# Performance work log

Hardware: AMD Instinct MI355X
Metric: run time of the kernel (lower is better)

The kernel has to match this reference:

```python
import jax, jax.numpy as jnp
import numpy as np

B, SEQ, IN, H = 256, 128, 512, 512


def setup_inputs() -> dict:
    key = jax.random.key(0)
    ks = jax.random.split(key, 7)
    s = 1.0 / np.sqrt(H)  # torch LSTM/Linear default init scale
    return {
        "x": jax.random.normal(ks[0], (B, SEQ, IN), dtype=jnp.float32),
        "W_ih": jax.random.uniform(ks[1], (4 * H, IN), jnp.float32, -s, s),
        "W_hh": jax.random.uniform(ks[2], (4 * H, H), jnp.float32, -s, s),
        "b_ih": jax.random.uniform(ks[3], (4 * H,), jnp.float32, -s, s),
        "b_hh": jax.random.uniform(ks[4], (4 * H,), jnp.float32, -s, s),
        "Wa": jax.random.uniform(ks[5], (SEQ, H), jnp.float32, -s, s),
        "ba": jax.random.uniform(ks[6], (SEQ,), jnp.float32, -s, s),
    }


def _lstm_cell(xi, h, c, W_ih, W_hh, b):
    # torch gate order: input, forget, cell(g), output
    gates = xi @ W_ih.T + h @ W_hh.T + b  # [B, 4H]
    i, f, g, o = jnp.split(gates, 4, axis=-1)
    c_new = jax.nn.sigmoid(f) * c + jax.nn.sigmoid(i) * jnp.tanh(g)
    h_new = jax.nn.sigmoid(o) * jnp.tanh(c_new)
    return h_new, c_new


def reference(x, W_ih, W_hh, b_ih, b_hh, Wa, ba):
    b = b_ih + b_hh
    bs, seq = x.shape[0], Wa.shape[0]
    h = jnp.zeros((bs, W_hh.shape[1]), x.dtype)
    c = jnp.zeros_like(h)
    # initial step on zero input (x[:,0]*0), zero initial state
    h, c = _lstm_cell(jnp.zeros((bs, x.shape[2]), x.dtype), h, c, W_ih, W_hh, b)

    def step(carry, _):
        h, c = carry
        attn = jax.nn.softmax(c @ Wa.T + ba, axis=-1)      # [B, seq]
        xi = jnp.einsum('bs,bsd->bd', attn, x)             # attention-weighted input
        h, c = _lstm_cell(xi, h, c, W_ih, W_hh, b)
        return (h, c), h

    _, hs = jax.lax.scan(step, (h, c), None, length=seq)   # [seq, B, H]
    return jnp.transpose(hs, (1, 0, 2))                    # [B, seq, H]
```

## Files before the change

kernel.cpp:

```cpp
#include <hip/hip_runtime.h>
#include <stdint.h>

#define BDIM 256
#define SEQL 128
#define IND 512
#define HID 512
#define KDIM 1024

typedef __bf16 bf16x8 __attribute__((ext_vector_type(8)));
typedef float floatx4 __attribute__((ext_vector_type(4)));
typedef _Float16 f16x8 __attribute__((ext_vector_type(8)));

__device__ __forceinline__ float sigm(float x) { return 1.0f / (1.0f + __expf(-x)); }

__device__ __forceinline__ ushort f2bf(float v) {
  uint32_t x = __builtin_bit_cast(uint32_t, v);
  x += 0x7fffu + ((x >> 16) & 1u);
  return (ushort)(x >> 16);
}
__device__ __forceinline__ float bf2f(ushort u) {
  return __builtin_bit_cast(float, ((uint32_t)u) << 16);
}

__global__ __launch_bounds__(256) void k_wconv(
    const float* __restrict__ W_ih, const float* __restrict__ W_hh,
    const float* __restrict__ b_ih, const float* __restrict__ b_hh,
    ushort* __restrict__ Whi, ushort* __restrict__ Wlo, float* __restrict__ bias) {
  int row = blockIdx.x;
  if (threadIdx.x == 0) bias[row] = b_ih[row] + b_hh[row];
  for (int k = threadIdx.x; k < KDIM; k += 256) {
    float w = (k < IND) ? W_ih[(size_t)row * IND + k] : W_hh[(size_t)row * HID + (k - IND)];
    ushort hi = f2bf(w);
    Whi[(size_t)row * KDIM + k] = hi;
    Wlo[(size_t)row * KDIM + k] = f2bf(w - bf2f(hi));
  }
}

__global__ __launch_bounds__(256) void k_xconv(const float* __restrict__ x,
                                               _Float16* __restrict__ xh) {
  size_t i = ((size_t)blockIdx.x * 256 + threadIdx.x) * 8;
  float4 v0 = *(const float4*)(x + i);
  float4 v1 = *(const float4*)(x + i + 4);
  f16x8 o;
  o[0] = (_Float16)v0.x; o[1] = (_Float16)v0.y; o[2] = (_Float16)v0.z; o[3] = (_Float16)v0.w;
  o[4] = (_Float16)v1.x; o[5] = (_Float16)v1.y; o[6] = (_Float16)v1.z; o[7] = (_Float16)v1.w;
  *(f16x8*)(xh + i) = o;
}

__global__ void k_init(const float* __restrict__ b_ih, const float* __restrict__ b_hh,
                       float* __restrict__ c, ushort* __restrict__ Ahi, ushort* __restrict__ Alo) {
  int b = blockIdx.x;
  for (int j = threadIdx.x; j < HID; j += blockDim.x) {
    float bi = b_ih[j] + b_hh[j];
    float bg = b_ih[2 * HID + j] + b_hh[2 * HID + j];
    float bo = b_ih[3 * HID + j] + b_hh[3 * HID + j];
    float c0 = sigm(bi) * tanhf(bg);
    float h0 = sigm(bo) * tanhf(c0);
    c[b * HID + j] = c0;
    ushort hi = f2bf(h0);
    Ahi[(size_t)b * KDIM + IND + j] = hi;
    Alo[(size_t)b * KDIM + IND + j] = f2bf(h0 - bf2f(hi));
  }
}

__global__ __launch_bounds__(256) void k_attn(const float* __restrict__ c, const float* __restrict__ Wa,
                                              const float* __restrict__ ba, const _Float16* __restrict__ xh,
                                              ushort* __restrict__ Ahi, ushort* __restrict__ Alo) {
  __shared__ float sc[HID];
  __shared__ float sl[SEQL];
  __shared__ float sxi[4][HID];
  int b = blockIdx.x, tid = threadIdx.x;
  sc[tid] = c[b * HID + tid];
  sc[tid + 256] = c[b * HID + tid + 256];
  __syncthreads();
  int wave = tid >> 6, lane = tid & 63;
  float4 c0 = *(const float4*)(&sc[lane * 4]);
  float4 c1 = *(const float4*)(&sc[lane * 4 + 256]);
#pragma unroll 4
  for (int si = 0; si < 32; ++si) {
    int s = wave * 32 + si;
    const float4* wr = (const float4*)(Wa + (size_t)s * HID);
    float4 w0 = wr[lane];
    float4 w1 = wr[lane + 64];
    float acc = c0.x * w0.x + c0.y * w0.y + c0.z * w0.z + c0.w * w0.w
              + c1.x * w1.x + c1.y * w1.y + c1.z * w1.z + c1.w * w1.w;
#pragma unroll
    for (int off = 32; off > 0; off >>= 1) acc += __shfl_down(acc, off);
    if (lane == 0) sl[s] = acc + ba[s];
  }
  __syncthreads();
  if (tid < 64) {
    float v0 = sl[tid], v1 = sl[tid + 64];
    float m = fmaxf(v0, v1);
#pragma unroll
    for (int off = 32; off > 0; off >>= 1) m = fmaxf(m, __shfl_xor(m, off));
    float e0 = __expf(v0 - m), e1 = __expf(v1 - m);
    float s2 = e0 + e1;
#pragma unroll
    for (int off = 32; off > 0; off >>= 1) s2 += __shfl_xor(s2, off);
    float inv = 1.f / s2;
    sl[tid] = e0 * inv; sl[tid + 64] = e1 * inv;
  }
  __syncthreads();
  int cix = tid & 63;
  int qp = tid >> 6;
  const _Float16* xrow = xh + (size_t)b * SEQL * IND + (size_t)qp * 32 * IND + 8 * cix;
  float a0 = 0.f, a1 = 0.f, a2 = 0.f, a3 = 0.f, a4 = 0.f, a5 = 0.f, a6 = 0.f, a7 = 0.f;
#pragma unroll 8
  for (int s = 0; s < 32; ++s) {
    float w = sl[qp * 32 + s];
    f16x8 v = *(const f16x8*)(xrow + (size_t)s * IND);
    a0 += w * (float)v[0]; a1 += w * (float)v[1];
    a2 += w * (float)v[2]; a3 += w * (float)v[3];
    a4 += w * (float)v[4]; a5 += w * (float)v[5];
    a6 += w * (float)v[6]; a7 += w * (float)v[7];
  }
  *(float4*)(&sxi[qp][8 * cix])     = (float4){a0, a1, a2, a3};
  *(float4*)(&sxi[qp][8 * cix + 4]) = (float4){a4, a5, a6, a7};
  __syncthreads();
  float rx = sxi[0][2 * tid] + sxi[1][2 * tid] + sxi[2][2 * tid] + sxi[3][2 * tid];
  float ry = sxi[0][2 * tid + 1] + sxi[1][2 * tid + 1] + sxi[2][2 * tid + 1] + sxi[3][2 * tid + 1];
  ushort hx = f2bf(rx), hy = f2bf(ry);
  uint hp = (uint)hx | ((uint)hy << 16);
  uint lp = (uint)f2bf(rx - bf2f(hx)) | ((uint)f2bf(ry - bf2f(hy)) << 16);
  *(uint*)(Ahi + (size_t)b * KDIM + 2 * tid) = hp;
  *(uint*)(Alo + (size_t)b * KDIM + 2 * tid) = lp;
}

#define G3LOAD(R, KO) do { \
  R##a  = *(const uint4*)(gA + (KO)); \
  R##w0 = *(const uint4*)(gWhi + (KO));      R##w1 = *(const uint4*)(gWhi + (KO) + 8);  \
  R##w2 = *(const uint4*)(gWlo + (KO));      R##w3 = *(const uint4*)(gWlo + (KO) + 8);  } while (0)
#define G3STORE(BUF, R) do { \
  *(uint4*)&sA[BUF][sthalf][ar][ac] = R##a; \
  *(uint4*)&sW[BUF][0][wr][wc] = R##w0;  *(uint4*)&sW[BUF][0][wr][wc + 8] = R##w1; \
  *(uint4*)&sW[BUF][1][wr][wc] = R##w2;  *(uint4*)&sW[BUF][1][wr][wc + 8] = R##w3; } while (0)
#define G3COMPUTE(BUF) do { \
  _Pragma("unroll") for (int ks = 0; ks < 2; ++ks) { \
    int kb = ks * 32 + koff; \
    bf16x8 ah = *(const bf16x8*)(&sA[BUF][0][ml][kb]); \
    bf16x8 al = *(const bf16x8*)(&sA[BUF][1][ml][kb]); \
    bf16x8 wh = *(const bf16x8*)(&sW[BUF][0][g * 16 + ml][kb]); \
    bf16x8 wl = *(const bf16x8*)(&sW[BUF][1][g * 16 + ml][kb]); \
    accA = __builtin_amdgcn_mfma_f32_16x16x32_bf16(ah, wh, accA, 0, 0, 0); \
    accB = __builtin_amdgcn_mfma_f32_16x16x32_bf16(ah, wl, accB, 0, 0, 0); \
    accB = __builtin_amdgcn_mfma_f32_16x16x32_bf16(al, wh, accB, 0, 0, 0); } } while (0)

__global__ __launch_bounds__(256) void k_gates(
    const ushort* __restrict__ Whi, const ushort* __restrict__ Wlo,
    const float* __restrict__ bias,
    const ushort* __restrict__ Ahi, const ushort* __restrict__ Alo,
    float* __restrict__ c, float* __restrict__ out,
    ushort* __restrict__ Dhi, ushort* __restrict__ Dlo, int tstep) {
  int bid = blockIdx.x;
  int lb = (bid & 7) * 64 + (bid >> 3);
  int j0 = (lb >> 4) * 16;
  int b0 = (lb & 15) * 16;

  __shared__ __align__(16) ushort sA[2][2][16][72];
  __shared__ __align__(16) ushort sW[2][2][64][72];
  __shared__ float sR[4][16][16];

  int tid = threadIdx.x;
  int sthalf = tid >> 7;
  int ar = (tid & 127) >> 3;
  int ac = (tid & 7) * 8;
  const ushort* gA = (sthalf ? Alo : Ahi) + (size_t)(b0 + ar) * KDIM + ac;
  int wr = tid >> 2;
  int wc = (tid & 3) * 16;
  int wrow = (wr >> 4) * HID + j0 + (wr & 15);
  const ushort* gWhi = Whi + (size_t)wrow * KDIM + wc;
  const ushort* gWlo = Wlo + (size_t)wrow * KDIM + wc;

  floatx4 accA = {0.f, 0.f, 0.f, 0.f}, accB = {0.f, 0.f, 0.f, 0.f};
  int lane = tid & 63, g = tid >> 6;
  int ml = lane & 15;
  int koff = (lane >> 4) * 8;

  uint4 Aa, Aw0, Aw1, Aw2, Aw3;
  uint4 Ba, Bw0, Bw1, Bw2, Bw3;

  G3LOAD(A, 0);
  G3LOAD(B, 64);
  G3STORE(0, A);
  G3STORE(1, B);
  G3LOAD(A, 128);
  G3LOAD(B, 192);
  __syncthreads();

  for (int k0 = 0; k0 < 16; k0 += 2) {
    G3COMPUTE(0);
    __syncthreads();
    if (k0 + 2 < 16) {
      G3STORE(0, A);
      if (k0 + 4 < 16) G3LOAD(A, (k0 + 4) * 64);
    }
    G3COMPUTE(1);
    __syncthreads();
    if (k0 + 3 < 16) {
      G3STORE(1, B);
      if (k0 + 5 < 16) G3LOAD(B, (k0 + 5) * 64);
    }
  }

  {
    floatx4 acc = accA + accB;
#pragma unroll
    for (int r = 0; r < 4; ++r) sR[g][ml][(lane >> 4) * 4 + r] = acc[r];
  }
  __syncthreads();

  {
    int jj = tid & 15, bb = tid >> 4;
    int jg = j0 + jj;
    int b = b0 + bb;
    float ig = sigm(sR[0][jj][bb] + bias[jg]);
    float fg = sigm(sR[1][jj][bb] + bias[HID + jg]);
    float gg = tanhf(sR[2][jj][bb] + bias[2 * HID + jg]);
    float og = sigm(sR[3][jj][bb] + bias[3 * HID + jg]);
    float co = c[b * HID + jg];
    float cn = fg * co + ig * gg;
    float hv = og * tanhf(cn);
    c[b * HID + jg] = cn;
    out[((size_t)b * SEQL + tstep) * HID + jg] = hv;
    ushort hi = f2bf(hv);
    Dhi[(size_t)b * KDIM + IND + jg] = hi;
    Dlo[(size_t)b * KDIM + IND + jg] = f2bf(hv - bf2f(hi));
  }
}

extern "C" void kernel_launch(void* const* d_in, const int* in_sizes, int n_in,
                              void* d_out, int out_size, void* d_ws, size_t ws_size,
                              hipStream_t stream) {
  (void)in_sizes; (void)n_in; (void)out_size; (void)ws_size;
  const float* x    = (const float*)d_in[0];
  const float* W_ih = (const float*)d_in[1];
  const float* W_hh = (const float*)d_in[2];
  const float* b_ih = (const float*)d_in[3];
  const float* b_hh = (const float*)d_in[4];
  const float* Wa   = (const float*)d_in[5];
  const float* ba   = (const float*)d_in[6];
  float* out = (float*)d_out;

  char* p = (char*)d_ws;
  auto carve = [&](size_t bytes) { char* r = p; p += (bytes + 255) & ~(size_t)255; return r; };
  float*  c    = (float*)carve((size_t)BDIM * HID * 4);
  float*  bias = (float*)carve((size_t)4 * HID * 4);
  ushort* Whi  = (ushort*)carve((size_t)4 * HID * KDIM * 2);
  ushort* Wlo  = (ushort*)carve((size_t)4 * HID * KDIM * 2);
  ushort* A0hi = (ushort*)carve((size_t)BDIM * KDIM * 2);
  ushort* A0lo = (ushort*)carve((size_t)BDIM * KDIM * 2);
  ushort* A1hi = (ushort*)carve((size_t)BDIM * KDIM * 2);
  ushort* A1lo = (ushort*)carve((size_t)BDIM * KDIM * 2);
  _Float16* xh = (_Float16*)carve((size_t)BDIM * SEQL * IND * 2);

  k_wconv<<<4 * HID, 256, 0, stream>>>(W_ih, W_hh, b_ih, b_hh, Whi, Wlo, bias);
  k_xconv<<<(BDIM * SEQL * IND) / (256 * 8), 256, 0, stream>>>(x, xh);
  k_init<<<BDIM, 256, 0, stream>>>(b_ih, b_hh, c, A0hi, A0lo);

  for (int t = 0; t < SEQL; ++t) {
    ushort* Rhi = (t & 1) ? A1hi : A0hi;
    ushort* Rlo = (t & 1) ? A1lo : A0lo;
    ushort* Dhi = (t & 1) ? A0hi : A1hi;
    ushort* Dlo = (t & 1) ? A0lo : A1lo;
    k_attn<<<BDIM, 256, 0, stream>>>(c, Wa, ba, xh, Rhi, Rlo);
    k_gates<<<512, 256, 0, stream>>>(Whi, Wlo, bias, Rhi, Rlo, c, out, Dhi, Dlo, t);
  }
}
```

Baseline: 4.707 ms.

## Fuse attention and gate kernels per step with per-tile atomic barrier

Merges the per-timestep attention kernel and gate GEMM kernel into one launch of 256 blocks. Each block first computes the attention-weighted input for one batch row. It then waits on an atomic counter shared by the 16 blocks of its batch tile, and finally computes gates for 16 batch rows by 32 hidden units. The aim is to halve kernel launches and the gaps between them, and to halve reloads of the activation tile by doubling each block's weight tile. The cost is a spin barrier that assumes all blocks are co-resident, plus fewer blocks for the GEMM phase.

```diff
diff --git a/kernel.cpp b/kernel.cpp
--- a/kernel.cpp
+++ b/kernel.cpp
@@ -63,169 +63,198 @@
   }
 }
 
-__global__ __launch_bounds__(256) void k_attn(const float* __restrict__ c, const float* __restrict__ Wa,
-                                              const float* __restrict__ ba, const _Float16* __restrict__ xh,
-                                              ushort* __restrict__ Ahi, ushort* __restrict__ Alo) {
-  __shared__ float sc[HID];
-  __shared__ float sl[SEQL];
-  __shared__ float sxi[4][HID];
-  int b = blockIdx.x, tid = threadIdx.x;
-  sc[tid] = c[b * HID + tid];
-  sc[tid + 256] = c[b * HID + tid + 256];
+struct AttnS { float sc[HID]; float sl[SEQL]; float sxi[4][HID]; };
+struct GateS {
+  ushort sA[2][2][16][72];
+  ushort sW[2][2][2][64][72];
+  float  sR[2][4][16][16];
+};
+union SU { AttnS a; GateS g; };
+
+__device__ __forceinline__ void gsync(unsigned* cnt, unsigned target) {
   __syncthreads();
-  int wave = tid >> 6, lane = tid & 63;
-  float4 c0 = *(const float4*)(&sc[lane * 4]);
-  float4 c1 = *(const float4*)(&sc[lane * 4 + 256]);
-#pragma unroll 4
-  for (int si = 0; si < 32; ++si) {
-    int s = wave * 32 + si;
-    const float4* wr = (const float4*)(Wa + (size_t)s * HID);
-    float4 w0 = wr[lane];
-    float4 w1 = wr[lane + 64];
-    float acc = c0.x * w0.x + c0.y * w0.y + c0.z * w0.z + c0.w * w0.w
-              + c1.x * w1.x + c1.y * w1.y + c1.z * w1.z + c1.w * w1.w;
-#pragma unroll
-    for (int off = 32; off > 0; off >>= 1) acc += __shfl_down(acc, off);
-    if (lane == 0) sl[s] = acc + ba[s];
+  if (threadIdx.x == 0) {
+    __hip_atomic_fetch_add(cnt, 1u, __ATOMIC_RELEASE, __HIP_MEMORY_SCOPE_AGENT);
+    while (__hip_atomic_load(cnt, __ATOMIC_RELAXED, __HIP_MEMORY_SCOPE_AGENT) < target)
+      __builtin_amdgcn_s_sleep(4);
+    (void)__hip_atomic_load(cnt, __ATOMIC_ACQUIRE, __HIP_MEMORY_SCOPE_AGENT);
   }
   __syncthreads();
-  if (tid < 64) {
-    float v0 = sl[tid], v1 = sl[tid + 64];
-    float m = fmaxf(v0, v1);
-#pragma unroll
-    for (int off = 32; off > 0; off >>= 1) m = fmaxf(m, __shfl_xor(m, off));
-    float e0 = __expf(v0 - m), e1 = __expf(v1 - m);
-    float s2 = e0 + e1;
-#pragma unroll
-    for (int off = 32; off > 0; off >>= 1) s2 += __shfl_xor(s2, off);
-    float inv = 1.f / s2;
-    sl[tid] = e0 * inv; sl[tid + 64] = e1 * inv;
-  }
-  __syncthreads();
-  int cix = tid & 63;
-  int qp = tid >> 6;
-  const _Float16* xrow = xh + (size_t)b * SEQL * IND + (size_t)qp * 32 * IND + 8 * cix;
-  float a0 = 0.f, a1 = 0.f, a2 = 0.f, a3 = 0.f, a4 = 0.f, a5 = 0.f, a6 = 0.f, a7 = 0.f;
-#pragma unroll 8
-  for (int s = 0; s < 32; ++s) {
-    float w = sl[qp * 32 + s];
-    f16x8 v = *(const f16x8*)(xrow + (size_t)s * IND);
-    a0 += w * (float)v[0]; a1 += w * (float)v[1];
-    a2 += w * (float)v[2]; a3 += w * (float)v[3];
-    a4 += w * (float)v[4]; a5 += w * (float)v[5];
-    a6 += w * (float)v[6]; a7 += w * (float)v[7];
-  }
-  *(float4*)(&sxi[qp][8 * cix])     = (float4){a0, a1, a2, a3};
-  *(float4*)(&sxi[qp][8 * cix + 4]) = (float4){a4, a5, a6, a7};
-  __syncthreads();
-  float rx = sxi[0][2 * tid] + sxi[1][2 * tid] + sxi[2][2 * tid] + sxi[3][2 * tid];
-  float ry = sxi[0][2 * tid + 1] + sxi[1][2 * tid + 1] + sxi[2][2 * tid + 1] + sxi[3][2 * tid + 1];
-  ushort hx = f2bf(rx), hy = f2bf(ry);
-  uint hp = (uint)hx | ((uint)hy << 16);
-  uint lp = (uint)f2bf(rx - bf2f(hx)) | ((uint)f2bf(ry - bf2f(hy)) << 16);
-  *(uint*)(Ahi + (size_t)b * KDIM + 2 * tid) = hp;
-  *(uint*)(Alo + (size_t)b * KDIM + 2 * tid) = lp;
-}
-
-#define G3LOAD(R, KO) do { \
-  R##a  = *(const uint4*)(gA + (KO)); \
-  R##w0 = *(const uint4*)(gWhi + (KO));      R##w1 = *(const uint4*)(gWhi + (KO) + 8);  \
-  R##w2 = *(const uint4*)(gWlo + (KO));      R##w3 = *(const uint4*)(gWlo + (KO) + 8);  } while (0)
-#define G3STORE(BUF, R) do { \
-  *(uint4*)&sA[BUF][sthalf][ar][ac] = R##a; \
-  *(uint4*)&sW[BUF][0][wr][wc] = R##w0;  *(uint4*)&sW[BUF][0][wr][wc + 8] = R##w1; \
-  *(uint4*)&sW[BUF][1][wr][wc] = R##w2;  *(uint4*)&sW[BUF][1][wr][wc + 8] = R##w3; } while (0)
-#define G3COMPUTE(BUF) do { \
+}
+
+#define MLOAD(R, KO) do { \
+  R##a   = *(const uint4*)(gA + (KO)); \
+  R##w00 = *(const uint4*)(gW0hi + (KO)); R##w01 = *(const uint4*)(gW0hi + (KO) + 8); \
+  R##w02 = *(const uint4*)(gW0lo + (KO)); R##w03 = *(const uint4*)(gW0lo + (KO) + 8); \
+  R##w10 = *(const uint4*)(gW1hi + (KO)); R##w11 = *(const uint4*)(gW1hi + (KO) + 8); \
+  R##w12 = *(const uint4*)(gW1lo + (KO)); R##w13 = *(const uint4*)(gW1lo + (KO) + 8); } while (0)
+#define MSTORE(BUF, R) do { \
+  *(uint4*)&su.g.sA[BUF][sthalf][ar][ac] = R##a; \
+  *(uint4*)&su.g.sW[BUF][0][0][wr][wc] = R##w00; *(uint4*)&su.g.sW[BUF][0][0][wr][wc + 8] = R##w01; \
+  *(uint4*)&su.g.sW[BUF][0][1][wr][wc] = R##w02; *(uint4*)&su.g.sW[BUF][0][1][wr][wc + 8] = R##w03; \
+  *(uint4*)&su.g.sW[BUF][1][0][wr][wc] = R##w10; *(uint4*)&su.g.sW[BUF][1][0][wr][wc + 8] = R##w11; \
+  *(uint4*)&su.g.sW[BUF][1][1][wr][wc] = R##w12; *(uint4*)&su.g.sW[BUF][1][1][wr][wc + 8] = R##w13; } while (0)
+#define MCOMPUTE(BUF) do { \
   _Pragma("unroll") for (int ks = 0; ks < 2; ++ks) { \
     int kb = ks * 32 + koff; \
-    bf16x8 ah = *(const bf16x8*)(&sA[BUF][0][ml][kb]); \
-    bf16x8 al = *(const bf16x8*)(&sA[BUF][1][ml][kb]); \
-    bf16x8 wh = *(const bf16x8*)(&sW[BUF][0][g * 16 + ml][kb]); \
-    bf16x8 wl = *(const bf16x8*)(&sW[BUF][1][g * 16 + ml][kb]); \
-    accA = __builtin_amdgcn_mfma_f32_16x16x32_bf16(ah, wh, accA, 0, 0, 0); \
-    accB = __builtin_amdgcn_mfma_f32_16x16x32_bf16(ah, wl, accB, 0, 0, 0); \
-    accB = __builtin_amdgcn_mfma_f32_16x16x32_bf16(al, wh, accB, 0, 0, 0); } } while (0)
-
-__global__ __launch_bounds__(256) void k_gates(
+    bf16x8 ah = *(const bf16x8*)(&su.g.sA[BUF][0][ml][kb]); \
+    bf16x8 al = *(const bf16x8*)(&su.g.sA[BUF][1][ml][kb]); \
+    bf16x8 wh0 = *(const bf16x8*)(&su.g.sW[BUF][0][0][g * 16 + ml][kb]); \
+    bf16x8 wl0 = *(const bf16x8*)(&su.g.sW[BUF][0][1][g * 16 + ml][kb]); \
+    bf16x8 wh1 = *(const bf16x8*)(&su.g.sW[BUF][1][0][g * 16 + ml][kb]); \
+    bf16x8 wl1 = *(const bf16x8*)(&su.g.sW[BUF][1][1][g * 16 + ml][kb]); \
+    acc0A = __builtin_amdgcn_mfma_f32_16x16x32_bf16(ah, wh0, acc0A, 0, 0, 0); \
+    acc1A = __builtin_amdgcn_mfma_f32_16x16x32_bf16(ah, wh1, acc1A, 0, 0, 0); \
+    acc0B = __builtin_amdgcn_mfma_f32_16x16x32_bf16(ah, wl0, acc0B, 0, 0, 0); \
+    acc0B = __builtin_amdgcn_mfma_f32_16x16x32_bf16(al, wh0, acc0B, 0, 0, 0); \
+    acc1B = __builtin_amdgcn_mfma_f32_16x16x32_bf16(ah, wl1, acc1B, 0, 0, 0); \
+    acc1B = __builtin_amdgcn_mfma_f32_16x16x32_bf16(al, wh1, acc1B, 0, 0, 0); } } while (0)
+
+__global__ __launch_bounds__(256) void k_step(
+    float* __restrict__ c, const float* __restrict__ Wa,
+    const float* __restrict__ ba, const _Float16* __restrict__ xh,
     const ushort* __restrict__ Whi, const ushort* __restrict__ Wlo,
     const float* __restrict__ bias,
-    const ushort* __restrict__ Ahi, const ushort* __restrict__ Alo,
-    float* __restrict__ c, float* __restrict__ out,
-    ushort* __restrict__ Dhi, ushort* __restrict__ Dlo, int tstep) {
-  int bid = blockIdx.x;
-  int lb = (bid & 7) * 64 + (bid >> 3);
-  int j0 = (lb >> 4) * 16;
-  int b0 = (lb & 15) * 16;
-
-  __shared__ __align__(16) ushort sA[2][2][16][72];
-  __shared__ __align__(16) ushort sW[2][2][64][72];
-  __shared__ float sR[4][16][16];
-
-  int tid = threadIdx.x;
-  int sthalf = tid >> 7;
-  int ar = (tid & 127) >> 3;
-  int ac = (tid & 7) * 8;
-  const ushort* gA = (sthalf ? Alo : Ahi) + (size_t)(b0 + ar) * KDIM + ac;
-  int wr = tid >> 2;
-  int wc = (tid & 3) * 16;
-  int wrow = (wr >> 4) * HID + j0 + (wr & 15);
-  const ushort* gWhi = Whi + (size_t)wrow * KDIM + wc;
-  const ushort* gWlo = Wlo + (size_t)wrow * KDIM + wc;
-
-  floatx4 accA = {0.f, 0.f, 0.f, 0.f}, accB = {0.f, 0.f, 0.f, 0.f};
-  int lane = tid & 63, g = tid >> 6;
-  int ml = lane & 15;
-  int koff = (lane >> 4) * 8;
-
-  uint4 Aa, Aw0, Aw1, Aw2, Aw3;
-  uint4 Ba, Bw0, Bw1, Bw2, Bw3;
-
-  G3LOAD(A, 0);
-  G3LOAD(B, 64);
-  G3STORE(0, A);
-  G3STORE(1, B);
-  G3LOAD(A, 128);
-  G3LOAD(B, 192);
-  __syncthreads();
-
-  for (int k0 = 0; k0 < 16; k0 += 2) {
-    G3COMPUTE(0);
-    __syncthreads();
-    if (k0 + 2 < 16) {
-      G3STORE(0, A);
-      if (k0 + 4 < 16) G3LOAD(A, (k0 + 4) * 64);
-    }
-    G3COMPUTE(1);
-    __syncthreads();
-    if (k0 + 3 < 16) {
-      G3STORE(1, B);
-      if (k0 + 5 < 16) G3LOAD(B, (k0 + 5) * 64);
-    }
-  }
+    const ushort* __restrict__ Rhi, const ushort* __restrict__ Rlo,
+    ushort* __restrict__ Dhi, ushort* __restrict__ Dlo,
+    float* __restrict__ out, unsigned* __restrict__ bar, int t) {
+  __shared__ __align__(16) SU su;
+  int blk = blockIdx.x, tid = threadIdx.x;
+  int lane = tid & 63, wave = tid >> 6;
+  int n = blk & 7, s = blk >> 3;
+  int bt = s & 15, psel = s >> 4;
+  int b0 = bt * 16;
+  int myb = b0 + 2 * n + psel;
+  int j0a = (4 * n + 2 * psel) * 16;
+  int j0b = j0a + 16;
 
   {
-    floatx4 acc = accA + accB;
-#pragma unroll
-    for (int r = 0; r < 4; ++r) sR[g][ml][(lane >> 4) * 4 + r] = acc[r];
-  }
-  __syncthreads();
+    su.a.sc[tid] = c[myb * HID + tid];
+    su.a.sc[tid + 256] = c[myb * HID + tid + 256];
+    __syncthreads();
+    float4 c0 = *(const float4*)(&su.a.sc[lane * 4]);
+    float4 c1 = *(const float4*)(&su.a.sc[lane * 4 + 256]);
+#pragma unroll 4
+    for (int si = 0; si < 32; ++si) {
+      int ss = wave * 32 + si;
+      const float4* wr4 = (const float4*)(Wa + (size_t)ss * HID);
+      float4 w0 = wr4[lane];
+      float4 w1 = wr4[lane + 64];
+      float acc = c0.x * w0.x + c0.y * w0.y + c0.z * w0.z + c0.w * w0.w
+                + c1.x * w1.x + c1.y * w1.y + c1.z * w1.z + c1.w * w1.w;
+#pragma unroll
+      for (int off = 32; off > 0; off >>= 1) acc += __shfl_down(acc, off);
+      if (lane == 0) su.a.sl[ss] = acc + ba[ss];
+    }
+    __syncthreads();
+    if (tid < 64) {
+      float v0 = su.a.sl[tid], v1 = su.a.sl[tid + 64];
+      float m = fmaxf(v0, v1);
+#pragma unroll
+      for (int off = 32; off > 0; off >>= 1) m = fmaxf(m, __shfl_xor(m, off));
+      float e0 = __expf(v0 - m), e1 = __expf(v1 - m);
+      float s2 = e0 + e1;
+#pragma unroll
+      for (int off = 32; off > 0; off >>= 1) s2 += __shfl_xor(s2, off);
+      float inv = 1.f / s2;
+      su.a.sl[tid] = e0 * inv; su.a.sl[tid + 64] = e1 * inv;
+    }
+    __syncthreads();
+    int cix = tid & 63, qp = tid >> 6;
+    const _Float16* xrow = xh + (size_t)myb * SEQL * IND + (size_t)qp * 32 * IND + 8 * cix;
+    float a0 = 0.f, a1 = 0.f, a2 = 0.f, a3 = 0.f, a4 = 0.f, a5 = 0.f, a6 = 0.f, a7 = 0.f;
+#pragma unroll 8
+    for (int ss = 0; ss < 32; ++ss) {
+      float w = su.a.sl[qp * 32 + ss];
+      f16x8 v = *(const f16x8*)(xrow + (size_t)ss * IND);
+      a0 += w * (float)v[0]; a1 += w * (float)v[1];
+      a2 += w * (float)v[2]; a3 += w * (float)v[3];
+      a4 += w * (float)v[4]; a5 += w * (float)v[5];
+      a6 += w * (float)v[6]; a7 += w * (float)v[7];
+    }
+    *(float4*)(&su.a.sxi[qp][8 * cix])     = (float4){a0, a1, a2, a3};
+    *(float4*)(&su.a.sxi[qp][8 * cix + 4]) = (float4){a4, a5, a6, a7};
+    __syncthreads();
+    float rx = su.a.sxi[0][2 * tid] + su.a.sxi[1][2 * tid] + su.a.sxi[2][2 * tid] + su.a.sxi[3][2 * tid];
+    float ry = su.a.sxi[0][2 * tid + 1] + su.a.sxi[1][2 * tid + 1] + su.a.sxi[2][2 * tid + 1] + su.a.sxi[3][2 * tid + 1];
+    ushort hx = f2bf(rx), hy = f2bf(ry);
+    uint hp = (uint)hx | ((uint)hy << 16);
+    uint lp = (uint)f2bf(rx - bf2f(hx)) | ((uint)f2bf(ry - bf2f(hy)) << 16);
+    *(uint*)(const_cast<ushort*>(Rhi) + (size_t)myb * KDIM + 2 * tid) = hp;
+    *(uint*)(const_cast<ushort*>(Rlo) + (size_t)myb * KDIM + 2 * tid) = lp;
+  }
+
+  gsync(bar + bt * 16, 16u * (unsigned)(t + 1));
 
   {
+    int sthalf = tid >> 7;
+    int ar = (tid & 127) >> 3, ac = (tid & 7) * 8;
+    const ushort* gA = (sthalf ? Rlo : Rhi) + (size_t)(b0 + ar) * KDIM + ac;
+    int wr = tid >> 2, wc = (tid & 3) * 16;
+    int wrow0 = (wr >> 4) * HID + j0a + (wr & 15);
+    const ushort* gW0hi = Whi + (size_t)wrow0 * KDIM + wc;
+    const ushort* gW0lo = Wlo + (size_t)wrow0 * KDIM + wc;
+    const ushort* gW1hi = Whi + (size_t)(wrow0 + 16) * KDIM + wc;
+    const ushort* gW1lo = Wlo + (size_t)(wrow0 + 16) * KDIM + wc;
+
+    floatx4 acc0A = {0.f, 0.f, 0.f, 0.f}, acc0B = {0.f, 0.f, 0.f, 0.f};
+    floatx4 acc1A = {0.f, 0.f, 0.f, 0.f}, acc1B = {0.f, 0.f, 0.f, 0.f};
+    int g = tid >> 6, ml = lane & 15, koff = (lane >> 4) * 8;
+
+    uint4 Aa, Aw00, Aw01, Aw02, Aw03, Aw10, Aw11, Aw12, Aw13;
+    uint4 Ba, Bw00, Bw01, Bw02, Bw03, Bw10, Bw11, Bw12, Bw13;
+
+    MLOAD(A, 0);
+    MLOAD(B, 64);
+    MSTORE(0, A);
+    MSTORE(1, B);
+    MLOAD(A, 128);
+    MLOAD(B, 192);
+    __syncthreads();
+
+    for (int k0 = 0; k0 < 16; k0 += 2) {
+      MCOMPUTE(0);
+      __syncthreads();
+      if (k0 + 2 < 16) {
+        MSTORE(0, A);
+        if (k0 + 4 < 16) MLOAD(A, (k0 + 4) * 64);
+      }
+      MCOMPUTE(1);
+      __syncthreads();
+      if (k0 + 3 < 16) {
+        MSTORE(1, B);
+        if (k0 + 5 < 16) MLOAD(B, (k0 + 5) * 64);
+      }
+    }
+
+    {
+      floatx4 r0 = acc0A + acc0B, r1 = acc1A + acc1B;
+#pragma unroll
+      for (int r = 0; r < 4; ++r) {
+        su.g.sR[0][g][ml][(lane >> 4) * 4 + r] = r0[r];
+        su.g.sR[1][g][ml][(lane >> 4) * 4 + r] = r1[r];
+      }
+    }
+    __syncthreads();
+
     int jj = tid & 15, bb = tid >> 4;
-    int jg = j0 + jj;
-    int b = b0 + bb;
-    float ig = sigm(sR[0][jj][bb] + bias[jg]);
-    float fg = sigm(sR[1][jj][bb] + bias[HID + jg]);
-    float gg = tanhf(sR[2][jj][bb] + bias[2 * HID + jg]);
-    float og = sigm(sR[3][jj][bb] + bias[3 * HID + jg]);
-    float co = c[b * HID + jg];
-    float cn = fg * co + ig * gg;
-    float hv = og * tanhf(cn);
-    c[b * HID + jg] = cn;
-    out[((size_t)b * SEQL + tstep) * HID + jg] = hv;
-    ushort hi = f2bf(hv);
-    Dhi[(size_t)b * KDIM + IND + jg] = hi;
-    Dlo[(size_t)b * KDIM + IND + jg] = f2bf(hv - bf2f(hi));
+#pragma unroll
+    for (int t2 = 0; t2 < 2; ++t2) {
+      int jg = (t2 ? j0b : j0a) + jj;
+      int b = b0 + bb;
+      float ig = sigm(su.g.sR[t2][0][jj][bb] + bias[jg]);
+      float fg = sigm(su.g.sR[t2][1][jj][bb] + bias[HID + jg]);
+      float gg = tanhf(su.g.sR[t2][2][jj][bb] + bias[2 * HID + jg]);
+      float og = sigm(su.g.sR[t2][3][jj][bb] + bias[3 * HID + jg]);
+      float co = c[b * HID + jg];
+      float cn = fg * co + ig * gg;
+      float hv = og * tanhf(cn);
+      c[b * HID + jg] = cn;
+      out[((size_t)b * SEQL + t) * HID + jg] = hv;
+      ushort hi = f2bf(hv);
+      Dhi[(size_t)b * KDIM + IND + jg] = hi;
+      Dlo[(size_t)b * KDIM + IND + jg] = f2bf(hv - bf2f(hi));
+    }
   }
 }
 
@@ -244,6 +273,7 @@
 
   char* p = (char*)d_ws;
   auto carve = [&](size_t bytes) { char* r = p; p += (bytes + 255) & ~(size_t)255; return r; };
+  unsigned* bar = (unsigned*)carve(1024);
   float*  c    = (float*)carve((size_t)BDIM * HID * 4);
   float*  bias = (float*)carve((size_t)4 * HID * 4);
   ushort* Whi  = (ushort*)carve((size_t)4 * HID * KDIM * 2);
@@ -254,6 +284,7 @@
   ushort* A1lo = (ushort*)carve((size_t)BDIM * KDIM * 2);
   _Float16* xh = (_Float16*)carve((size_t)BDIM * SEQL * IND * 2);
 
+  hipMemsetAsync(bar, 0, 1024, stream);
   k_wconv<<<4 * HID, 256, 0, stream>>>(W_ih, W_hh, b_ih, b_hh, Whi, Wlo, bias);
   k_xconv<<<(BDIM * SEQL * IND) / (256 * 8), 256, 0, stream>>>(x, xh);
   k_init<<<BDIM, 256, 0, stream>>>(b_ih, b_hh, c, A0hi, A0lo);
@@ -263,7 +294,7 @@
     ushort* Rlo = (t & 1) ? A1lo : A0lo;
     ushort* Dhi = (t & 1) ? A0hi : A1hi;
     ushort* Dlo = (t & 1) ? A0lo : A1lo;
-    k_attn<<<BDIM, 256, 0, stream>>>(c, Wa, ba, xh, Rhi, Rlo);
-    k_gates<<<512, 256, 0, stream>>>(Whi, Wlo, bias, Rhi, Rlo, c, out, Dhi, Dlo, t);
-  }
-}
+    k_step<<<256, 256, 0, stream>>>(c, Wa, ba, xh, Whi, Wlo, bias,
+                                    Rhi, Rlo, Dhi, Dlo, out, bar, t);
+  }
+}
```

Result: slower. 5.175 ms (+9.9%).

## Split gate GEMM so recurrent half runs concurrently with attention

Applied to the files above, without the earlier changes.

The per-step gate GEMM is split by K. The h·W_hh half (K=512..1023) now runs in the same launch as the attention kernel, using extra blocks that write partial sums to a workspace buffer. The second kernel then computes only the x·W_ih half, adds the stored partials, and applies the LSTM cell update. This fills the GPU during the small 256-block attention kernel and halves the K-loop on the critical path after attention. The cost is a partial-sum buffer round trip through global memory and a larger shared-memory union in both kernels.

```diff
diff --git a/kernel.cpp b/kernel.cpp
--- a/kernel.cpp
+++ b/kernel.cpp
@@ -63,150 +63,164 @@
   }
 }
 
-__global__ __launch_bounds__(256) void k_attn(const float* __restrict__ c, const float* __restrict__ Wa,
-                                              const float* __restrict__ ba, const _Float16* __restrict__ xh,
-                                              ushort* __restrict__ Ahi, ushort* __restrict__ Alo) {
-  __shared__ float sc[HID];
-  __shared__ float sl[SEQL];
-  __shared__ float sxi[4][HID];
-  int b = blockIdx.x, tid = threadIdx.x;
-  sc[tid] = c[b * HID + tid];
-  sc[tid + 256] = c[b * HID + tid + 256];
-  __syncthreads();
-  int wave = tid >> 6, lane = tid & 63;
-  float4 c0 = *(const float4*)(&sc[lane * 4]);
-  float4 c1 = *(const float4*)(&sc[lane * 4 + 256]);
-#pragma unroll 4
-  for (int si = 0; si < 32; ++si) {
-    int s = wave * 32 + si;
-    const float4* wr = (const float4*)(Wa + (size_t)s * HID);
-    float4 w0 = wr[lane];
-    float4 w1 = wr[lane + 64];
-    float acc = c0.x * w0.x + c0.y * w0.y + c0.z * w0.z + c0.w * w0.w
-              + c1.x * w1.x + c1.y * w1.y + c1.z * w1.z + c1.w * w1.w;
-#pragma unroll
-    for (int off = 32; off > 0; off >>= 1) acc += __shfl_down(acc, off);
-    if (lane == 0) sl[s] = acc + ba[s];
-  }
-  __syncthreads();
-  if (tid < 64) {
-    float v0 = sl[tid], v1 = sl[tid + 64];
-    float m = fmaxf(v0, v1);
-#pragma unroll
-    for (int off = 32; off > 0; off >>= 1) m = fmaxf(m, __shfl_xor(m, off));
-    float e0 = __expf(v0 - m), e1 = __expf(v1 - m);
-    float s2 = e0 + e1;
-#pragma unroll
-    for (int off = 32; off > 0; off >>= 1) s2 += __shfl_xor(s2, off);
-    float inv = 1.f / s2;
-    sl[tid] = e0 * inv; sl[tid + 64] = e1 * inv;
-  }
-  __syncthreads();
-  int cix = tid & 63;
-  int qp = tid >> 6;
-  const _Float16* xrow = xh + (size_t)b * SEQL * IND + (size_t)qp * 32 * IND + 8 * cix;
-  float a0 = 0.f, a1 = 0.f, a2 = 0.f, a3 = 0.f, a4 = 0.f, a5 = 0.f, a6 = 0.f, a7 = 0.f;
-#pragma unroll 8
-  for (int s = 0; s < 32; ++s) {
-    float w = sl[qp * 32 + s];
-    f16x8 v = *(const f16x8*)(xrow + (size_t)s * IND);
-    a0 += w * (float)v[0]; a1 += w * (float)v[1];
-    a2 += w * (float)v[2]; a3 += w * (float)v[3];
-    a4 += w * (float)v[4]; a5 += w * (float)v[5];
-    a6 += w * (float)v[6]; a7 += w * (float)v[7];
-  }
-  *(float4*)(&sxi[qp][8 * cix])     = (float4){a0, a1, a2, a3};
-  *(float4*)(&sxi[qp][8 * cix + 4]) = (float4){a4, a5, a6, a7};
-  __syncthreads();
-  float rx = sxi[0][2 * tid] + sxi[1][2 * tid] + sxi[2][2 * tid] + sxi[3][2 * tid];
-  float ry = sxi[0][2 * tid + 1] + sxi[1][2 * tid + 1] + sxi[2][2 * tid + 1] + sxi[3][2 * tid + 1];
-  ushort hx = f2bf(rx), hy = f2bf(ry);
-  uint hp = (uint)hx | ((uint)hy << 16);
-  uint lp = (uint)f2bf(rx - bf2f(hx)) | ((uint)f2bf(ry - bf2f(hy)) << 16);
-  *(uint*)(Ahi + (size_t)b * KDIM + 2 * tid) = hp;
-  *(uint*)(Alo + (size_t)b * KDIM + 2 * tid) = lp;
-}
+struct AttnS { float sc[HID]; float sl[SEQL]; float sxi[4][HID]; };
+struct GemmS {
+  ushort sA[2][2][16][72];
+  ushort sW[2][2][64][72];
+  float  sR[4][16][16];
+};
+union SU { AttnS a; GemmS g; };
 
 #define G3LOAD(R, KO) do { \
   R##a  = *(const uint4*)(gA + (KO)); \
   R##w0 = *(const uint4*)(gWhi + (KO));      R##w1 = *(const uint4*)(gWhi + (KO) + 8);  \
   R##w2 = *(const uint4*)(gWlo + (KO));      R##w3 = *(const uint4*)(gWlo + (KO) + 8);  } while (0)
 #define G3STORE(BUF, R) do { \
-  *(uint4*)&sA[BUF][sthalf][ar][ac] = R##a; \
-  *(uint4*)&sW[BUF][0][wr][wc] = R##w0;  *(uint4*)&sW[BUF][0][wr][wc + 8] = R##w1; \
-  *(uint4*)&sW[BUF][1][wr][wc] = R##w2;  *(uint4*)&sW[BUF][1][wr][wc + 8] = R##w3; } while (0)
+  *(uint4*)&su.g.sA[BUF][sthalf][ar][ac] = R##a; \
+  *(uint4*)&su.g.sW[BUF][0][wr][wc] = R##w0;  *(uint4*)&su.g.sW[BUF][0][wr][wc + 8] = R##w1; \
+  *(uint4*)&su.g.sW[BUF][1][wr][wc] = R##w2;  *(uint4*)&su.g.sW[BUF][1][wr][wc + 8] = R##w3; } while (0)
 #define G3COMPUTE(BUF) do { \
   _Pragma("unroll") for (int ks = 0; ks < 2; ++ks) { \
     int kb = ks * 32 + koff; \
-    bf16x8 ah = *(const bf16x8*)(&sA[BUF][0][ml][kb]); \
-    bf16x8 al = *(const bf16x8*)(&sA[BUF][1][ml][kb]); \
-    bf16x8 wh = *(const bf16x8*)(&sW[BUF][0][g * 16 + ml][kb]); \
-    bf16x8 wl = *(const bf16x8*)(&sW[BUF][1][g * 16 + ml][kb]); \
+    bf16x8 ah = *(const bf16x8*)(&su.g.sA[BUF][0][ml][kb]); \
+    bf16x8 al = *(const bf16x8*)(&su.g.sA[BUF][1][ml][kb]); \
+    bf16x8 wh = *(const bf16x8*)(&su.g.sW[BUF][0][g * 16 + ml][kb]); \
+    bf16x8 wl = *(const bf16x8*)(&su.g.sW[BUF][1][g * 16 + ml][kb]); \
     accA = __builtin_amdgcn_mfma_f32_16x16x32_bf16(ah, wh, accA, 0, 0, 0); \
     accB = __builtin_amdgcn_mfma_f32_16x16x32_bf16(ah, wl, accB, 0, 0, 0); \
     accB = __builtin_amdgcn_mfma_f32_16x16x32_bf16(al, wh, accB, 0, 0, 0); } } while (0)
-
-__global__ __launch_bounds__(256) void k_gates(
+#define G3LOOP(NCH) \
+  G3LOAD(A, 0); G3LOAD(B, 64); \
+  G3STORE(0, A); G3STORE(1, B); \
+  G3LOAD(A, 128); G3LOAD(B, 192); \
+  __syncthreads(); \
+  for (int k0 = 0; k0 < (NCH); k0 += 2) { \
+    G3COMPUTE(0); \
+    __syncthreads(); \
+    if (k0 + 2 < (NCH)) { G3STORE(0, A); if (k0 + 4 < (NCH)) G3LOAD(A, (k0 + 4) * 64); } \
+    G3COMPUTE(1); \
+    __syncthreads(); \
+    if (k0 + 3 < (NCH)) { G3STORE(1, B); if (k0 + 5 < (NCH)) G3LOAD(B, (k0 + 5) * 64); } \
+  }
+
+__global__ __launch_bounds__(256) void k1_attn_gatesH(
+    const float* __restrict__ c, const float* __restrict__ Wa,
+    const float* __restrict__ ba, const _Float16* __restrict__ xh,
     const ushort* __restrict__ Whi, const ushort* __restrict__ Wlo,
-    const float* __restrict__ bias,
-    const ushort* __restrict__ Ahi, const ushort* __restrict__ Alo,
+    ushort* __restrict__ Rhi, ushort* __restrict__ Rlo,
+    float* __restrict__ P) {
+  __shared__ __align__(16) SU su;
+  int blk = blockIdx.x, tid = threadIdx.x;
+  int lane = tid & 63, wave = tid >> 6;
+
+  if (blk < 256) {
+    int b = blk;
+    su.a.sc[tid] = c[b * HID + tid];
+    su.a.sc[tid + 256] = c[b * HID + tid + 256];
+    __syncthreads();
+    float4 c0 = *(const float4*)(&su.a.sc[lane * 4]);
+    float4 c1 = *(const float4*)(&su.a.sc[lane * 4 + 256]);
+#pragma unroll 4
+    for (int si = 0; si < 32; ++si) {
+      int s = wave * 32 + si;
+      const float4* wr4 = (const float4*)(Wa + (size_t)s * HID);
+      float4 w0 = wr4[lane];
+      float4 w1 = wr4[lane + 64];
+      float acc = c0.x * w0.x + c0.y * w0.y + c0.z * w0.z + c0.w * w0.w
+                + c1.x * w1.x + c1.y * w1.y + c1.z * w1.z + c1.w * w1.w;
+#pragma unroll
+      for (int off = 32; off > 0; off >>= 1) acc += __shfl_down(acc, off);
+      if (lane == 0) su.a.sl[s] = acc + ba[s];
+    }
+    __syncthreads();
+    if (tid < 64) {
+      float v0 = su.a.sl[tid], v1 = su.a.sl[tid + 64];
+      float m = fmaxf(v0, v1);
+#pragma unroll
+      for (int off = 32; off > 0; off >>= 1) m = fmaxf(m, __shfl_xor(m, off));
+      float e0 = __expf(v0 - m), e1 = __expf(v1 - m);
+      float s2 = e0 + e1;
+#pragma unroll
+      for (int off = 32; off > 0; off >>= 1) s2 += __shfl_xor(s2, off);
+      float inv = 1.f / s2;
+      su.a.sl[tid] = e0 * inv; su.a.sl[tid + 64] = e1 * inv;
+    }
+    __syncthreads();
+    int cix = tid & 63, qp = tid >> 6;
+    const _Float16* xrow = xh + (size_t)b * SEQL * IND + (size_t)qp * 32 * IND + 8 * cix;
+    float a0 = 0.f, a1 = 0.f, a2 = 0.f, a3 = 0.f, a4 = 0.f, a5 = 0.f, a6 = 0.f, a7 = 0.f;
+#pragma unroll 8
+    for (int s = 0; s < 32; ++s) {
+      float w = su.a.sl[qp * 32 + s];
+      f16x8 v = *(const f16x8*)(xrow + (size_t)s * IND);
+      a0 += w * (float)v[0]; a1 += w * (float)v[1];
+      a2 += w * (float)v[2]; a3 += w * (float)v[3];
+      a4 += w * (float)v[4]; a5 += w * (float)v[5];
+      a6 += w * (float)v[6]; a7 += w * (float)v[7];
+    }
+    *(float4*)(&su.a.sxi[qp][8 * cix])     = (float4){a0, a1, a2, a3};
+    *(float4*)(&su.a.sxi[qp][8 * cix + 4]) = (float4){a4, a5, a6, a7};
+    __syncthreads();
+    float rx = su.a.sxi[0][2 * tid] + su.a.sxi[1][2 * tid] + su.a.sxi[2][2 * tid] + su.a.sxi[3][2 * tid];
+    float ry = su.a.sxi[0][2 * tid + 1] + su.a.sxi[1][2 * tid + 1] + su.a.sxi[2][2 * tid + 1] + su.a.sxi[3][2 * tid + 1];
+    ushort hx = f2bf(rx), hy = f2bf(ry);
+    uint hp = (uint)hx | ((uint)hy << 16);
+    uint lp = (uint)f2bf(rx - bf2f(hx)) | ((uint)f2bf(ry - bf2f(hy)) << 16);
+    *(uint*)(Rhi + (size_t)b * KDIM + 2 * tid) = hp;
+    *(uint*)(Rlo + (size_t)b * KDIM + 2 * tid) = lp;
+  } else {
+    int g2 = blk - 256;
+    int lb = (g2 & 7) * 64 + (g2 >> 3);
+    int j0 = (lb >> 4) * 16;
+    int b0 = (lb & 15) * 16;
+    int sthalf = tid >> 7;
+    int ar = (tid & 127) >> 3, ac = (tid & 7) * 8;
+    const ushort* gA = (sthalf ? Rlo : Rhi) + (size_t)(b0 + ar) * KDIM + IND + ac;
+    int wr = tid >> 2, wc = (tid & 3) * 16;
+    int wrow = (wr >> 4) * HID + j0 + (wr & 15);
+    const ushort* gWhi = Whi + (size_t)wrow * KDIM + IND + wc;
+    const ushort* gWlo = Wlo + (size_t)wrow * KDIM + IND + wc;
+
+    floatx4 accA = {0.f, 0.f, 0.f, 0.f}, accB = {0.f, 0.f, 0.f, 0.f};
+    int g = tid >> 6, ml = lane & 15, koff = (lane >> 4) * 8;
+    uint4 Aa, Aw0, Aw1, Aw2, Aw3, Ba, Bw0, Bw1, Bw2, Bw3;
+    G3LOOP(8)
+
+    floatx4 acc = accA + accB;
+    size_t pbase = (((size_t)g * 32 + (j0 >> 4)) * 16 + (b0 >> 4)) * 256;
+    *(float4*)(P + pbase + ml * 16 + (lane >> 4) * 4) = *(float4*)&acc;
+  }
+}
+
+__global__ __launch_bounds__(256) void k2_gatesX(
+    const ushort* __restrict__ Whi, const ushort* __restrict__ Wlo,
+    const float* __restrict__ bias, const float* __restrict__ P,
+    const ushort* __restrict__ Rhi, const ushort* __restrict__ Rlo,
     float* __restrict__ c, float* __restrict__ out,
     ushort* __restrict__ Dhi, ushort* __restrict__ Dlo, int tstep) {
-  int bid = blockIdx.x;
+  __shared__ __align__(16) SU su;
+  int bid = blockIdx.x, tid = threadIdx.x;
+  int lane = tid & 63;
   int lb = (bid & 7) * 64 + (bid >> 3);
   int j0 = (lb >> 4) * 16;
   int b0 = (lb & 15) * 16;
-
-  __shared__ __align__(16) ushort sA[2][2][16][72];
-  __shared__ __align__(16) ushort sW[2][2][64][72];
-  __shared__ float sR[4][16][16];
-
-  int tid = threadIdx.x;
   int sthalf = tid >> 7;
-  int ar = (tid & 127) >> 3;
-  int ac = (tid & 7) * 8;
-  const ushort* gA = (sthalf ? Alo : Ahi) + (size_t)(b0 + ar) * KDIM + ac;
-  int wr = tid >> 2;
-  int wc = (tid & 3) * 16;
+  int ar = (tid & 127) >> 3, ac = (tid & 7) * 8;
+  const ushort* gA = (sthalf ? Rlo : Rhi) + (size_t)(b0 + ar) * KDIM + ac;
+  int wr = tid >> 2, wc = (tid & 3) * 16;
   int wrow = (wr >> 4) * HID + j0 + (wr & 15);
   const ushort* gWhi = Whi + (size_t)wrow * KDIM + wc;
   const ushort* gWlo = Wlo + (size_t)wrow * KDIM + wc;
 
   floatx4 accA = {0.f, 0.f, 0.f, 0.f}, accB = {0.f, 0.f, 0.f, 0.f};
-  int lane = tid & 63, g = tid >> 6;
-  int ml = lane & 15;
-  int koff = (lane >> 4) * 8;
-
-  uint4 Aa, Aw0, Aw1, Aw2, Aw3;
-  uint4 Ba, Bw0, Bw1, Bw2, Bw3;
-
-  G3LOAD(A, 0);
-  G3LOAD(B, 64);
-  G3STORE(0, A);
-  G3STORE(1, B);
-  G3LOAD(A, 128);
-  G3LOAD(B, 192);
-  __syncthreads();
-
-  for (int k0 = 0; k0 < 16; k0 += 2) {
-    G3COMPUTE(0);
-    __syncthreads();
-    if (k0 + 2 < 16) {
-      G3STORE(0, A);
-      if (k0 + 4 < 16) G3LOAD(A, (k0 + 4) * 64);
-    }
-    G3COMPUTE(1);
-    __syncthreads();
-    if (k0 + 3 < 16) {
-      G3STORE(1, B);
-      if (k0 + 5 < 16) G3LOAD(B, (k0 + 5) * 64);
-    }
-  }
+  int g = tid >> 6, ml = lane & 15, koff = (lane >> 4) * 8;
+  uint4 Aa, Aw0, Aw1, Aw2, Aw3, Ba, Bw0, Bw1, Bw2, Bw3;
+  G3LOOP(8)
 
   {
     floatx4 acc = accA + accB;
 #pragma unroll
-    for (int r = 0; r < 4; ++r) sR[g][ml][(lane >> 4) * 4 + r] = acc[r];
+    for (int r = 0; r < 4; ++r) su.g.sR[g][ml][(lane >> 4) * 4 + r] = acc[r];
   }
   __syncthreads();
 
@@ -214,10 +228,12 @@
     int jj = tid & 15, bb = tid >> 4;
     int jg = j0 + jj;
     int b = b0 + bb;
-    float ig = sigm(sR[0][jj][bb] + bias[jg]);
-    float fg = sigm(sR[1][jj][bb] + bias[HID + jg]);
-    float gg = tanhf(sR[2][jj][bb] + bias[2 * HID + jg]);
-    float og = sigm(sR[3][jj][bb] + bias[3 * HID + jg]);
+    size_t pb = (((size_t)(j0 >> 4)) * 16 + (b0 >> 4)) * 256 + jj * 16 + bb;
+    const size_t gstr = (size_t)32 * 16 * 256;
+    float ig = sigm(su.g.sR[0][jj][bb] + P[pb]            + bias[jg]);
+    float fg = sigm(su.g.sR[1][jj][bb] + P[pb + gstr]     + bias[HID + jg]);
+    float gg = tanhf(su.g.sR[2][jj][bb] + P[pb + 2 * gstr] + bias[2 * HID + jg]);
+    float og = sigm(su.g.sR[3][jj][bb] + P[pb + 3 * gstr] + bias[3 * HID + jg]);
     float co = c[b * HID + jg];
     float cn = fg * co + ig * gg;
     float hv = og * tanhf(cn);
@@ -253,6 +269,7 @@
   ushort* A1hi = (ushort*)carve((size_t)BDIM * KDIM * 2);
   ushort* A1lo = (ushort*)carve((size_t)BDIM * KDIM * 2);
   _Float16* xh = (_Float16*)carve((size_t)BDIM * SEQL * IND * 2);
+  float*  P    = (float*)carve((size_t)4 * HID * BDIM * 4);
 
   k_wconv<<<4 * HID, 256, 0, stream>>>(W_ih, W_hh, b_ih, b_hh, Whi, Wlo, bias);
   k_xconv<<<(BDIM * SEQL * IND) / (256 * 8), 256, 0, stream>>>(x, xh);
@@ -263,7 +280,7 @@
     ushort* Rlo = (t & 1) ? A1lo : A0lo;
     ushort* Dhi = (t & 1) ? A0hi : A1hi;
     ushort* Dlo = (t & 1) ? A0lo : A1lo;
-    k_attn<<<BDIM, 256, 0, stream>>>(c, Wa, ba, xh, Rhi, Rlo);
-    k_gates<<<512, 256, 0, stream>>>(Whi, Wlo, bias, Rhi, Rlo, c, out, Dhi, Dlo, t);
-  }
-}
+    k1_attn_gatesH<<<768, 256, 0, stream>>>(c, Wa, ba, xh, Whi, Wlo, Rhi, Rlo, P);
+    k2_gatesX<<<512, 256, 0, stream>>>(Whi, Wlo, bias, P, Rhi, Rlo, c, out, Dhi, Dlo, t);
+  }
+}
```

Measured after the change: 4.385 ms. 1.07x faster.
